# Kernel tuning notes

Measured on AMD Instinct MI355X. Metric: run time of the kernel, lower is better.

The kernel has to match this reference:

```python
import jax, jax.numpy as jnp
import numpy as np

F = 26  # num_sparse_features
N = F + 1
# upper-triangular (offset=1) index pairs, matching torch.triu_indices(N, N, offset=1)
_TRIU_I, _TRIU_J = np.triu_indices(N, k=1)


def setup_inputs() -> dict:
    key = jax.random.key(0)
    k1, k2 = jax.random.split(key)
    B, D = 16384, 128
    dense_features = jax.random.normal(k1, (B, D), dtype=jnp.float32)
    sparse_features = jax.random.normal(k2, (B, F, D), dtype=jnp.float32)
    return {"dense_features": dense_features, "sparse_features": sparse_features}


def reference(dense_features, sparse_features):
    # combined: [B, N, D] with N = F + 1 (dense row first)
    combined = jnp.concatenate([dense_features[:, None, :], sparse_features], axis=1)
    # pairwise dot products: [B, N, N]
    interactions = jnp.einsum('bnd,bmd->bnm', combined, combined)
    # gather strict upper triangle: [B, N*(N-1)/2]
    interactions_flat = interactions[:, _TRIU_I, _TRIU_J]
    # output: [B, D + F + F choose 2]
    return jnp.concatenate([dense_features, interactions_flat], axis=1)
```

## Files before the change

kernel.cpp:

```cpp
#include <hip/hip_runtime.h>


#define FEAT 26
#define NROW 27
#define DDIM 128
#define NTRI 351
#define OUTW 479
#define LDST 136

typedef _Float16 half2v __attribute__((ext_vector_type(2)));
typedef _Float16 half4v __attribute__((ext_vector_type(4)));
typedef _Float16 half8v __attribute__((ext_vector_type(8)));
typedef float    f32x16 __attribute__((ext_vector_type(16)));

__global__ __launch_bounds__(256) void interaction_kernel(
    const float* __restrict__ dense,
    const float* __restrict__ sparse,
    float* __restrict__ out)
{
    __shared__ _Float16 Xs[4][32][LDST];
    __shared__ float    Tri[4][NTRI + 1];

    const int lane = threadIdx.x & 63;
    const int w    = threadIdx.x >> 6;
    const long b   = (long)blockIdx.x * 4 + w;

    const float* dn   = dense  + b * DDIM;
    const float* sp   = sparse + b * (FEAT * DDIM);
    float*       orow = out    + b * OUTW;

    {
        float2 v = *(const float2*)(dn + lane * 2);
        orow[lane * 2 + 0] = v.x;
        orow[lane * 2 + 1] = v.y;
        half2v h;
        h.x = (_Float16)v.x; h.y = (_Float16)v.y;
        *(half2v*)(&Xs[w][0][lane * 2]) = h;
    }

#pragma unroll
    for (int t = 0; t < 13; ++t) {
        int idx = t * 64 + lane;
        float4 v = *(const float4*)(sp + idx * 4);
        int row = 1 + (idx >> 5);
        int col = (idx & 31) * 4;
        half4v h;
        h.x = (_Float16)v.x; h.y = (_Float16)v.y;
        h.z = (_Float16)v.z; h.w = (_Float16)v.w;
        *(half4v*)(&Xs[w][row][col]) = h;
    }
    __syncthreads();

    const int j0 = lane & 31;
    const int q  = lane >> 5;
    const half8v* fp = (const half8v*)(&Xs[w][j0][q * 8]);

    f32x16 acc = {0,0,0,0,0,0,0,0,0,0,0,0,0,0,0,0};
#pragma unroll
    for (int s = 0; s < 8; ++s) {
        half8v f = fp[2 * s];
        acc = __builtin_amdgcn_mfma_f32_32x32x16_f16(f, f, acc, 0, 0, 0);
    }

#pragma unroll
    for (int reg = 0; reg < 16; ++reg) {
        int row = (reg & 3) + 8 * (reg >> 2) + 4 * q;
        if (row < j0 && j0 < NROW) {
            int t = row * (2 * NROW - row - 1) / 2 + (j0 - row - 1);
            Tri[w][t] = acc[reg];
        }
    }
    __syncthreads();

    for (int idx = lane; idx < NTRI; idx += 64)
        orow[DDIM + idx] = Tri[w][idx];
}

extern "C" void kernel_launch(void* const* d_in, const int* in_sizes, int n_in,
                              void* d_out, int out_size, void* d_ws, size_t ws_size,
                              hipStream_t stream) {
    const float* dense  = (const float*)d_in[0];
    const float* sparse = (const float*)d_in[1];
    float* out = (float*)d_out;
    interaction_kernel<<<4096, 256, 0, stream>>>(dense, sparse, out);
}
```

Baseline: 311.6 us.

## Make waves persistent over batch rows and replace block barriers with wave barriers

The grid shrinks to 1024 blocks, and each wave loops over 4 batch rows strided by the total wave count. The block-wide __syncthreads calls become wave barriers plus LDS waitcnt, because each wave only touches its own shared slice. The aim is to cut launch and barrier overhead and let waves run independently. The risk is fewer resident waves to hide memory latency, and rows inside a wave are processed serially without prefetch.

```diff
diff --git a/kernel.cpp b/kernel.cpp
--- a/kernel.cpp
+++ b/kernel.cpp
@@ -7,73 +7,88 @@
 #define NTRI 351
 #define OUTW 479
 #define LDST 136
+#define WPB   4
+#define GRID  1024
+#define NWAVE (GRID * WPB)
+#define ITERS 4
 
 typedef _Float16 half2v __attribute__((ext_vector_type(2)));
 typedef _Float16 half4v __attribute__((ext_vector_type(4)));
 typedef _Float16 half8v __attribute__((ext_vector_type(8)));
 typedef float    f32x16 __attribute__((ext_vector_type(16)));
 
+#define LGKM0() __builtin_amdgcn_s_waitcnt(0xC07F)
+
 __global__ __launch_bounds__(256) void interaction_kernel(
     const float* __restrict__ dense,
     const float* __restrict__ sparse,
     float* __restrict__ out)
 {
-    __shared__ _Float16 Xs[4][32][LDST];
-    __shared__ float    Tri[4][NTRI + 1];
+    __shared__ _Float16 Xs[WPB][32][LDST];
+    __shared__ float    Tri[WPB][NTRI + 1];
 
     const int lane = threadIdx.x & 63;
     const int w    = threadIdx.x >> 6;
-    const long b   = (long)blockIdx.x * 4 + w;
-
-    const float* dn   = dense  + b * DDIM;
-    const float* sp   = sparse + b * (FEAT * DDIM);
-    float*       orow = out    + b * OUTW;
-
-    {
-        float2 v = *(const float2*)(dn + lane * 2);
-        orow[lane * 2 + 0] = v.x;
-        orow[lane * 2 + 1] = v.y;
-        half2v h;
-        h.x = (_Float16)v.x; h.y = (_Float16)v.y;
-        *(half2v*)(&Xs[w][0][lane * 2]) = h;
-    }
-
-#pragma unroll
-    for (int t = 0; t < 13; ++t) {
-        int idx = t * 64 + lane;
-        float4 v = *(const float4*)(sp + idx * 4);
-        int row = 1 + (idx >> 5);
-        int col = (idx & 31) * 4;
-        half4v h;
-        h.x = (_Float16)v.x; h.y = (_Float16)v.y;
-        h.z = (_Float16)v.z; h.w = (_Float16)v.w;
-        *(half4v*)(&Xs[w][row][col]) = h;
-    }
-    __syncthreads();
+    const int gw   = blockIdx.x * WPB + w;
 
     const int j0 = lane & 31;
     const int q  = lane >> 5;
     const half8v* fp = (const half8v*)(&Xs[w][j0][q * 8]);
 
-    f32x16 acc = {0,0,0,0,0,0,0,0,0,0,0,0,0,0,0,0};
-#pragma unroll
-    for (int s = 0; s < 8; ++s) {
-        half8v f = fp[2 * s];
-        acc = __builtin_amdgcn_mfma_f32_32x32x16_f16(f, f, acc, 0, 0, 0);
-    }
+    for (int it = 0; it < ITERS; ++it) {
+        const long b = gw + (long)it * NWAVE;
+        const float* dn   = dense  + b * DDIM;
+        const float* sp   = sparse + b * (FEAT * DDIM);
+        float*       orow = out    + b * OUTW;
+
+        {
+            float2 v = *(const float2*)(dn + lane * 2);
+            orow[lane * 2 + 0] = v.x;
+            orow[lane * 2 + 1] = v.y;
+            half2v h;
+            h.x = (_Float16)v.x; h.y = (_Float16)v.y;
+            *(half2v*)(&Xs[w][0][lane * 2]) = h;
+        }
 
 #pragma unroll
-    for (int reg = 0; reg < 16; ++reg) {
-        int row = (reg & 3) + 8 * (reg >> 2) + 4 * q;
-        if (row < j0 && j0 < NROW) {
-            int t = row * (2 * NROW - row - 1) / 2 + (j0 - row - 1);
-            Tri[w][t] = acc[reg];
+        for (int t = 0; t < 13; ++t) {
+            int idx = t * 64 + lane;
+            float4 v = *(const float4*)(sp + idx * 4);
+            int row = 1 + (idx >> 5);
+            int col = (idx & 31) * 4;
+            half4v h;
+            h.x = (_Float16)v.x; h.y = (_Float16)v.y;
+            h.z = (_Float16)v.z; h.w = (_Float16)v.w;
+            *(half4v*)(&Xs[w][row][col]) = h;
         }
+        __builtin_amdgcn_wave_barrier();
+        LGKM0();
+
+        f32x16 acc = {0,0,0,0,0,0,0,0,0,0,0,0,0,0,0,0};
+#pragma unroll
+        for (int s = 0; s < 8; ++s) {
+            half8v f = fp[2 * s];
+            acc = __builtin_amdgcn_mfma_f32_32x32x16_f16(f, f, acc, 0, 0, 0);
+        }
+
+#pragma unroll
+        for (int reg = 0; reg < 16; ++reg) {
+            int row = (reg & 3) + 8 * (reg >> 2) + 4 * q;
+            if (row < j0 && j0 < NROW) {
+                int t = row * (2 * NROW - row - 1) / 2 + (j0 - row - 1);
+                Tri[w][t] = acc[reg];
+            }
+        }
+        __builtin_amdgcn_wave_barrier();
+        LGKM0();
+
+#pragma unroll
+        for (int t = 0; t < 6; ++t) {
+            int idx = t * 64 + lane;
+            if (idx < NTRI) orow[DDIM + idx] = Tri[w][idx];
+        }
+        __builtin_amdgcn_wave_barrier();
     }
-    __syncthreads();
-
-    for (int idx = lane; idx < NTRI; idx += 64)
-        orow[DDIM + idx] = Tri[w][idx];
 }
 
 extern "C" void kernel_launch(void* const* d_in, const int* in_sizes, int n_in,
@@ -82,5 +97,5 @@
     const float* dense  = (const float*)d_in[0];
     const float* sparse = (const float*)d_in[1];
     float* out = (float*)d_out;
-    interaction_kernel<<<4096, 256, 0, stream>>>(dense, sparse, out);
+    interaction_kernel<<<GRID, 256, 0, stream>>>(dense, sparse, out);
 }
```

After: 311.9 us. No clear change (+0.1%).
